# Kernel tuning notes

Measured on AMD Instinct MI355X. Metric: run time of the kernel, lower is better.

## Reference

```python
import jax, jax.numpy as jnp
import numpy as np

IN_FEATURES = 2048
OUT_FEATURES = 8192


def ternary_quantize(w):
    # BitNet 1.58b: scale = mean(|w|), round to {-1,0,1}, rescale
    scale = jnp.mean(jnp.abs(w)) + 1e-8
    w_q = jnp.clip(jnp.round(w / scale), -1.0, 1.0)
    return w_q * scale


def setup_inputs() -> dict:
    key = jax.random.key(0)
    kx, kw = jax.random.split(key)
    x = jax.random.normal(kx, (4, 2048, IN_FEATURES), dtype=jnp.float32)
    # nn.init.normal_(std=1/sqrt(in_features))
    weight = jax.random.normal(kw, (OUT_FEATURES, IN_FEATURES), dtype=jnp.float32) / np.sqrt(IN_FEATURES)
    return {"x": x, "weight": weight}


def reference(x, weight):
    w = ternary_quantize(weight)
    # F.linear: x @ w.T  -> [B, S, out_features]
    return jnp.einsum('bsd,od->bso', x, w)
```

## Files before the change

kernel.cpp:

```cpp
#include <hip/hip_runtime.h>
#include <hip/hip_bf16.h>
#include <stdint.h>


typedef __attribute__((ext_vector_type(8))) short   s16x8;
typedef __attribute__((ext_vector_type(4))) float   f32x4;

#define K_DIM   2048
#define K2      4096
#define N_DIM   8192
#define N4      4194304

__global__ void k_abs_part(const float4* __restrict__ w4, float* __restrict__ part) {
    int tid = blockIdx.x * 256 + threadIdx.x;
    float s = 0.f;
    for (int i = tid; i < N4; i += gridDim.x * 256) {
        float4 v = w4[i];
        s += fabsf(v.x) + fabsf(v.y) + fabsf(v.z) + fabsf(v.w);
    }
    for (int off = 32; off > 0; off >>= 1) s += __shfl_down(s, off, 64);
    __shared__ float tmp[4];
    int lane = threadIdx.x & 63, wid = threadIdx.x >> 6;
    if (lane == 0) tmp[wid] = s;
    __syncthreads();
    if (threadIdx.x == 0) part[blockIdx.x] = tmp[0] + tmp[1] + tmp[2] + tmp[3];
}

__global__ void k_abs_final(const float* __restrict__ part, float* __restrict__ scale) {
    float s = part[threadIdx.x] + part[threadIdx.x + 256] +
              part[threadIdx.x + 512] + part[threadIdx.x + 768];
    for (int off = 32; off > 0; off >>= 1) s += __shfl_down(s, off, 64);
    __shared__ float tmp[4];
    int lane = threadIdx.x & 63, wid = threadIdx.x >> 6;
    if (lane == 0) tmp[wid] = s;
    __syncthreads();
    if (threadIdx.x == 0) scale[0] = (tmp[0] + tmp[1] + tmp[2] + tmp[3]) / 16777216.0f + 1e-8f;
}

__device__ __forceinline__ uint32_t f2b(float f) {
    uint32_t u = __builtin_bit_cast(uint32_t, f);
    return (u + 0x7FFFu + ((u >> 16) & 1u)) >> 16;
}

__global__ void k_prep(const float4* __restrict__ w4, const float4* __restrict__ x4,
                       const float* __restrict__ scale_p,
                       uint2* __restrict__ wq, uint2* __restrict__ xb) {
    int tid = (blockIdx.x & 2047) * 256 + threadIdx.x;
    if (blockIdx.x < 2048) {
        const float sc = *scale_p;
        for (int i = tid; i < N4; i += 2048 * 256) {
            float4 v = w4[i];
            float q0 = rintf(v.x / sc), q1 = rintf(v.y / sc);
            float q2 = rintf(v.z / sc), q3 = rintf(v.w / sc);
            uint32_t b0 = (q0 == 0.f) ? 0u : (q0 > 0.f ? 0x3F80u : 0xBF80u);
            uint32_t b1 = (q1 == 0.f) ? 0u : (q1 > 0.f ? 0x3F80u : 0xBF80u);
            uint32_t b2 = (q2 == 0.f) ? 0u : (q2 > 0.f ? 0x3F80u : 0xBF80u);
            uint32_t b3 = (q3 == 0.f) ? 0u : (q3 > 0.f ? 0x3F80u : 0xBF80u);
            uint2 o; o.x = b0 | (b1 << 16); o.y = b2 | (b3 << 16);
            wq[i] = o;
        }
    } else {
        for (int i = tid; i < N4; i += 2048 * 256) {
            float4 v = x4[i];
            uint2 o;
            o.x = f2b(v.x) | (f2b(v.y) << 16);
            o.y = f2b(v.z) | (f2b(v.w) << 16);
            xb[i] = o;
        }
    }
}

__device__ __forceinline__ void mfma16(f32x4& c, s16x8 a, s16x8 b) {
    asm("v_mfma_f32_16x16x32_bf16 %0, %1, %2, %0" : "+v"(c) : "v"(a), "v"(b));
}
__device__ __forceinline__ void load_lds16(const void* g, void* l) {
    __builtin_amdgcn_global_load_lds(
        (const __attribute__((address_space(1))) uint32_t*)g,
        (__attribute__((address_space(3))) uint32_t*)l, 16, 0, 0);
}

#define SCHED0 __builtin_amdgcn_sched_barrier(0)
#define SBAR do { SCHED0; __builtin_amdgcn_s_barrier(); SCHED0; } while (0)
#define WAIT_VM(N) do { asm volatile("s_waitcnt vmcnt(" #N ")" ::: "memory"); SCHED0; } while (0)

#define C0 0
#define C1 65536

__global__ __launch_bounds__(512, 2) void k_gemm(
    const unsigned short* __restrict__ Xb,
    const unsigned short* __restrict__ Wb,
    const float* __restrict__ scale_p,
    float* __restrict__ out)
{
    extern __shared__ uint8_t smem[];
    const int tid  = threadIdx.x;
    const int lane = tid & 63;
    const int wid  = tid >> 6;
    const int wr   = wid >> 2;
    const int wc   = wid & 3;

    const int bid = blockIdx.x;
    const int xcd = bid & 7;
    const int l   = bid >> 3;
    const int tileRow = xcd * 4 + ((l >> 3) & 3);
    const int tileCol = (l >> 5) * 8 + (l & 7);

    const uint8_t* gA = (const uint8_t*)Xb + (size_t)tileRow * 256 * K2;
    const uint8_t* gB = (const uint8_t*)Wb + (size_t)tileCol * 256 * K2;

    const int srow = tid >> 3, sslot = tid & 7;
    const size_t srcOff = (size_t)srow * K2 + (size_t)((sslot ^ (srow & 7)) * 16);
    const uint8_t* gAs = gA + srcOff;
    const uint8_t* gBs = gB + srcOff;
    const int dstOff = tid * 16;

    const int rA = wr * 128 + (lane & 15);
    const int rB = wc * 64  + (lane & 15);
    const int h  = lane >> 4;
    const int pA0 = rA * 128 + (((h    ) ^ (rA & 7)) * 16);
    const int pA1 = rA * 128 + (((4 + h) ^ (rA & 7)) * 16);
    const int pB0 = rB * 128 + (((h    ) ^ (rB & 7)) * 16);
    const int pB1 = rB * 128 + (((4 + h) ^ (rB & 7)) * 16);

    s16x8 a[8][2], b[4][2];
    f32x4 acc[8][4];
    #pragma unroll
    for (int m = 0; m < 8; ++m)
        #pragma unroll
        for (int n = 0; n < 4; ++n) acc[m][n] = (f32x4){0.f, 0.f, 0.f, 0.f};

#define LD8(OFF) (*(const s16x8*)(smem + (OFF)))
#define STAGE(LBASE, GP, BOFF) do { \
    load_lds16((GP) + (BOFF),          smem + (LBASE) + dstOff); \
    load_lds16((GP) + (BOFF) + 262144, smem + (LBASE) + 8192 + dstOff); \
    SCHED0; } while (0)

#define RD_A03(AB) do { _Pragma("unroll") for (int m = 0; m < 4; ++m) { \
    a[m][0] = LD8((AB) + pA0 + m * 2048); a[m][1] = LD8((AB) + pA1 + m * 2048); } } while (0)
#define RD_A47(AB) do { _Pragma("unroll") for (int m = 4; m < 8; ++m) { \
    a[m][0] = LD8((AB) + pA0 + m * 2048); a[m][1] = LD8((AB) + pA1 + m * 2048); } } while (0)
#define RD_B01(AB) do { _Pragma("unroll") for (int n = 0; n < 2; ++n) { \
    b[n][0] = LD8((AB) + 32768 + pB0 + n * 2048); b[n][1] = LD8((AB) + 32768 + pB1 + n * 2048); } } while (0)
#define RD_B23(AB) do { _Pragma("unroll") for (int n = 2; n < 4; ++n) { \
    b[n][0] = LD8((AB) + 32768 + pB0 + n * 2048); b[n][1] = LD8((AB) + 32768 + pB1 + n * 2048); } } while (0)

#define MFMA_Q(MLO, NLO) do { \
    __builtin_amdgcn_s_setprio(1); \
    _Pragma("unroll") for (int kk = 0; kk < 2; ++kk) \
        _Pragma("unroll") for (int m = 0; m < 4; ++m) \
            _Pragma("unroll") for (int n = 0; n < 2; ++n) \
                mfma16(acc[(MLO) + m][(NLO) + n], a[(MLO) + m][kk], b[(NLO) + n][kk]); \
    __builtin_amdgcn_s_setprio(0); \
    SCHED0; } while (0)

    STAGE(C0,         gAs, 0);   STAGE(C0 + 16384, gAs, 524288);
    STAGE(C0 + 32768, gBs, 0);   STAGE(C0 + 49152, gBs, 524288);
    STAGE(C1,         gAs, 128); STAGE(C1 + 16384, gAs, 524288 + 128);
    STAGE(C1 + 32768, gBs, 128); STAGE(C1 + 49152, gBs, 524288 + 128);
    WAIT_VM(8);
    SBAR;

    #pragma unroll 1
    for (int i = 0; i < 15; ++i) {
        const int kb1 = (2 * i + 1) * 128;
        const int kb2 = kb1 + 128;
        const int kb3 = kb1 + 256;
        STAGE(C1 + 32768, gBs, kb1);
        RD_A03(C0); RD_B01(C0);
        MFMA_Q(0, 0);
        STAGE(C1 + 49152, gBs, 524288 + kb1);
        RD_A47(C0);
        MFMA_Q(4, 0);
        SBAR;
        STAGE(C0, gAs, kb2);
        RD_B23(C0);
        MFMA_Q(0, 2);
        STAGE(C0 + 16384, gAs, 524288 + kb2);
        MFMA_Q(4, 2);
        WAIT_VM(4); SBAR;
        STAGE(C0 + 32768, gBs, kb2);
        RD_A03(C1); RD_B01(C1);
        MFMA_Q(0, 0);
        STAGE(C0 + 49152, gBs, 524288 + kb2);
        RD_A47(C1);
        MFMA_Q(4, 0);
        SBAR;
        STAGE(C1, gAs, kb3);
        RD_B23(C1);
        MFMA_Q(0, 2);
        STAGE(C1 + 16384, gAs, 524288 + kb3);
        MFMA_Q(4, 2);
        WAIT_VM(4); SBAR;
    }

    {
        const int kb1 = 31 * 128;
        STAGE(C1 + 32768, gBs, kb1);
        RD_A03(C0); RD_B01(C0);
        MFMA_Q(0, 0);
        STAGE(C1 + 49152, gBs, 524288 + kb1);
        RD_A47(C0);
        MFMA_Q(4, 0);
        SBAR;
        RD_B23(C0);
        MFMA_Q(0, 2);
        MFMA_Q(4, 2);
        WAIT_VM(0); SBAR;
        RD_A03(C1); RD_B01(C1);
        MFMA_Q(0, 0);
        RD_A47(C1);
        MFMA_Q(4, 0);
        RD_B23(C1);
        MFMA_Q(0, 2);
        MFMA_Q(4, 2);
    }

    const float sc = *scale_p;
    const int orow0 = tileRow * 256 + wr * 128 + ((lane >> 4) << 2);
    const int ocol0 = tileCol * 256 + wc * 64 + (lane & 15);
    #pragma unroll
    for (int m = 0; m < 8; ++m)
        #pragma unroll
        for (int n = 0; n < 4; ++n)
            #pragma unroll
            for (int j = 0; j < 4; ++j)
                out[(size_t)(orow0 + m * 16 + j) * N_DIM + (ocol0 + n * 16)] = acc[m][n][j] * sc;

#undef LD8
#undef STAGE
#undef RD_A03
#undef RD_A47
#undef RD_B01
#undef RD_B23
#undef MFMA_Q
}

extern "C" void kernel_launch(void* const* d_in, const int* in_sizes, int n_in,
                              void* d_out, int out_size, void* d_ws, size_t ws_size,
                              hipStream_t stream) {
    const float* x = (const float*)d_in[0];
    const float* w = (const float*)d_in[1];
    float* out = (float*)d_out;
    uint8_t* ws = (uint8_t*)d_ws;

    float* part  = (float*)ws;
    float* scale = (float*)(ws + 4096);
    unsigned short* Xb = (unsigned short*)(ws + 8192);
    unsigned short* Wb = (unsigned short*)(ws + 8192 + 33554432ull);

    (void)hipFuncSetAttribute((const void*)k_gemm,
                              hipFuncAttributeMaxDynamicSharedMemorySize, 131072);

    hipLaunchKernelGGL(k_abs_part, dim3(1024), dim3(256), 0, stream, (const float4*)w, part);
    hipLaunchKernelGGL(k_abs_final, dim3(1), dim3(256), 0, stream, part, scale);
    hipLaunchKernelGGL(k_prep, dim3(4096), dim3(256), 0, stream,
                       (const float4*)w, (const float4*)x, scale, (uint2*)Wb, (uint2*)Xb);
    hipLaunchKernelGGL(k_gemm, dim3(1024), dim3(512), 131072, stream, Xb, Wb, scale, out);
}
```

Before: 277.8 us.

## Shrink GEMM block tile to 128x128 with 4 waves and 64KB LDS

```diff
diff --git a/kernel.cpp b/kernel.cpp
--- a/kernel.cpp
+++ b/kernel.cpp
@@ -83,10 +83,12 @@
 #define SBAR do { SCHED0; __builtin_amdgcn_s_barrier(); SCHED0; } while (0)
 #define WAIT_VM(N) do { asm volatile("s_waitcnt vmcnt(" #N ")" ::: "memory"); SCHED0; } while (0)
 
-#define C0 0
-#define C1 65536
-
-__global__ __launch_bounds__(512, 2) void k_gemm(
+#define A0B 0
+#define B0B 16384
+#define A1B 32768
+#define B1B 49152
+
+__global__ __launch_bounds__(256, 2) void k_gemm(
     const unsigned short* __restrict__ Xb,
     const unsigned short* __restrict__ Wb,
     const float* __restrict__ scale_p,
@@ -96,17 +98,17 @@
     const int tid  = threadIdx.x;
     const int lane = tid & 63;
     const int wid  = tid >> 6;
-    const int wr   = wid >> 2;
-    const int wc   = wid & 3;
+    const int wr   = wid >> 1;
+    const int wc   = wid & 1;
 
     const int bid = blockIdx.x;
     const int xcd = bid & 7;
     const int l   = bid >> 3;
-    const int tileRow = xcd * 4 + ((l >> 3) & 3);
-    const int tileCol = (l >> 5) * 8 + (l & 7);
-
-    const uint8_t* gA = (const uint8_t*)Xb + (size_t)tileRow * 256 * K2;
-    const uint8_t* gB = (const uint8_t*)Wb + (size_t)tileCol * 256 * K2;
+    const int tileRow = xcd * 8 + (l & 7);
+    const int tileCol = l >> 3;
+
+    const uint8_t* gA = (const uint8_t*)Xb + (size_t)tileRow * 128 * K2;
+    const uint8_t* gB = (const uint8_t*)Wb + (size_t)tileCol * 128 * K2;
 
     const int srow = tid >> 3, sslot = tid & 7;
     const size_t srcOff = (size_t)srow * K2 + (size_t)((sslot ^ (srow & 7)) * 16);
@@ -114,50 +116,46 @@
     const uint8_t* gBs = gB + srcOff;
     const int dstOff = tid * 16;
 
-    const int rA = wr * 128 + (lane & 15);
-    const int rB = wc * 64  + (lane & 15);
+    const int rA = wr * 64 + (lane & 15);
+    const int rB = wc * 64 + (lane & 15);
     const int h  = lane >> 4;
     const int pA0 = rA * 128 + (((h    ) ^ (rA & 7)) * 16);
     const int pA1 = rA * 128 + (((4 + h) ^ (rA & 7)) * 16);
     const int pB0 = rB * 128 + (((h    ) ^ (rB & 7)) * 16);
     const int pB1 = rB * 128 + (((4 + h) ^ (rB & 7)) * 16);
 
-    s16x8 a[8][2], b[4][2];
-    f32x4 acc[8][4];
+    s16x8 a[4][2], b[4][2];
+    f32x4 acc[4][4];
     #pragma unroll
-    for (int m = 0; m < 8; ++m)
+    for (int m = 0; m < 4; ++m)
         #pragma unroll
         for (int n = 0; n < 4; ++n) acc[m][n] = (f32x4){0.f, 0.f, 0.f, 0.f};
 
 #define LD8(OFF) (*(const s16x8*)(smem + (OFF)))
 #define STAGE(LBASE, GP, BOFF) do { \
     load_lds16((GP) + (BOFF),          smem + (LBASE) + dstOff); \
-    load_lds16((GP) + (BOFF) + 262144, smem + (LBASE) + 8192 + dstOff); \
+    load_lds16((GP) + (BOFF) + 131072, smem + (LBASE) + 4096 + dstOff); \
     SCHED0; } while (0)
 
-#define RD_A03(AB) do { _Pragma("unroll") for (int m = 0; m < 4; ++m) { \
+#define RD_A(AB) do { _Pragma("unroll") for (int m = 0; m < 4; ++m) { \
     a[m][0] = LD8((AB) + pA0 + m * 2048); a[m][1] = LD8((AB) + pA1 + m * 2048); } } while (0)
-#define RD_A47(AB) do { _Pragma("unroll") for (int m = 4; m < 8; ++m) { \
-    a[m][0] = LD8((AB) + pA0 + m * 2048); a[m][1] = LD8((AB) + pA1 + m * 2048); } } while (0)
-#define RD_B01(AB) do { _Pragma("unroll") for (int n = 0; n < 2; ++n) { \
-    b[n][0] = LD8((AB) + 32768 + pB0 + n * 2048); b[n][1] = LD8((AB) + 32768 + pB1 + n * 2048); } } while (0)
-#define RD_B23(AB) do { _Pragma("unroll") for (int n = 2; n < 4; ++n) { \
-    b[n][0] = LD8((AB) + 32768 + pB0 + n * 2048); b[n][1] = LD8((AB) + 32768 + pB1 + n * 2048); } } while (0)
-
-#define MFMA_Q(MLO, NLO) do { \
+#define RD_B01(BB) do { _Pragma("unroll") for (int n = 0; n < 2; ++n) { \
+    b[n][0] = LD8((BB) + pB0 + n * 2048); b[n][1] = LD8((BB) + pB1 + n * 2048); } } while (0)
+#define RD_B23(BB) do { _Pragma("unroll") for (int n = 2; n < 4; ++n) { \
+    b[n][0] = LD8((BB) + pB0 + n * 2048); b[n][1] = LD8((BB) + pB1 + n * 2048); } } while (0)
+
+#define MFMA_Q(NLO, KC) do { \
     __builtin_amdgcn_s_setprio(1); \
-    _Pragma("unroll") for (int kk = 0; kk < 2; ++kk) \
-        _Pragma("unroll") for (int m = 0; m < 4; ++m) \
-            _Pragma("unroll") for (int n = 0; n < 2; ++n) \
-                mfma16(acc[(MLO) + m][(NLO) + n], a[(MLO) + m][kk], b[(NLO) + n][kk]); \
+    _Pragma("unroll") for (int m = 0; m < 4; ++m) \
+        _Pragma("unroll") for (int n = 0; n < 2; ++n) \
+            mfma16(acc[m][(NLO) + n], a[m][(KC)], b[(NLO) + n][(KC)]); \
     __builtin_amdgcn_s_setprio(0); \
     SCHED0; } while (0)
 
-    STAGE(C0,         gAs, 0);   STAGE(C0 + 16384, gAs, 524288);
-    STAGE(C0 + 32768, gBs, 0);   STAGE(C0 + 49152, gBs, 524288);
-    STAGE(C1,         gAs, 128); STAGE(C1 + 16384, gAs, 524288 + 128);
-    STAGE(C1 + 32768, gBs, 128); STAGE(C1 + 49152, gBs, 524288 + 128);
-    WAIT_VM(8);
+    STAGE(A0B, gAs, 0);   STAGE(A0B + 8192, gAs, 262144);
+    STAGE(B0B, gBs, 0);   STAGE(B0B + 8192, gBs, 262144);
+    STAGE(A1B, gAs, 128); STAGE(A1B + 8192, gAs, 262144 + 128);
+    WAIT_VM(4);
     SBAR;
 
     #pragma unroll 1
@@ -165,61 +163,57 @@
         const int kb1 = (2 * i + 1) * 128;
         const int kb2 = kb1 + 128;
         const int kb3 = kb1 + 256;
-        STAGE(C1 + 32768, gBs, kb1);
-        RD_A03(C0); RD_B01(C0);
-        MFMA_Q(0, 0);
-        STAGE(C1 + 49152, gBs, 524288 + kb1);
-        RD_A47(C0);
-        MFMA_Q(4, 0);
+        STAGE(B1B, gBs, kb1);
+        RD_A(A0B); RD_B01(B0B);
+        MFMA_Q(0, 0);
+        STAGE(B1B + 8192, gBs, 262144 + kb1);
+        RD_B23(B0B);
+        MFMA_Q(0, 1);
         SBAR;
-        STAGE(C0, gAs, kb2);
-        RD_B23(C0);
-        MFMA_Q(0, 2);
-        STAGE(C0 + 16384, gAs, 524288 + kb2);
-        MFMA_Q(4, 2);
+        STAGE(A0B, gAs, kb2);
+        MFMA_Q(2, 0);
+        STAGE(A0B + 8192, gAs, 262144 + kb2);
+        MFMA_Q(2, 1);
         WAIT_VM(4); SBAR;
-        STAGE(C0 + 32768, gBs, kb2);
-        RD_A03(C1); RD_B01(C1);
-        MFMA_Q(0, 0);
-        STAGE(C0 + 49152, gBs, 524288 + kb2);
-        RD_A47(C1);
-        MFMA_Q(4, 0);
+        STAGE(B0B, gBs, kb2);
+        RD_A(A1B); RD_B01(B1B);
+        MFMA_Q(0, 0);
+        STAGE(B0B + 8192, gBs, 262144 + kb2);
+        RD_B23(B1B);
+        MFMA_Q(0, 1);
         SBAR;
-        STAGE(C1, gAs, kb3);
-        RD_B23(C1);
-        MFMA_Q(0, 2);
-        STAGE(C1 + 16384, gAs, 524288 + kb3);
-        MFMA_Q(4, 2);
+        STAGE(A1B, gAs, kb3);
+        MFMA_Q(2, 0);
+        STAGE(A1B + 8192, gAs, 262144 + kb3);
+        MFMA_Q(2, 1);
         WAIT_VM(4); SBAR;
     }
 
     {
         const int kb1 = 31 * 128;
-        STAGE(C1 + 32768, gBs, kb1);
-        RD_A03(C0); RD_B01(C0);
-        MFMA_Q(0, 0);
-        STAGE(C1 + 49152, gBs, 524288 + kb1);
-        RD_A47(C0);
-        MFMA_Q(4, 0);
+        STAGE(B1B, gBs, kb1);
+        RD_A(A0B); RD_B01(B0B);
+        MFMA_Q(0, 0);
+        STAGE(B1B + 8192, gBs, 262144 + kb1);
+        RD_B23(B0B);
+        MFMA_Q(0, 1);
         SBAR;
-        RD_B23(C0);
-        MFMA_Q(0, 2);
-        MFMA_Q(4, 2);
+        MFMA_Q(2, 0);
+        MFMA_Q(2, 1);
         WAIT_VM(0); SBAR;
-        RD_A03(C1); RD_B01(C1);
-        MFMA_Q(0, 0);
-        RD_A47(C1);
-        MFMA_Q(4, 0);
-        RD_B23(C1);
-        MFMA_Q(0, 2);
-        MFMA_Q(4, 2);
+        RD_A(A1B); RD_B01(B1B);
+        MFMA_Q(0, 0);
+        RD_B23(B1B);
+        MFMA_Q(0, 1);
+        MFMA_Q(2, 0);
+        MFMA_Q(2, 1);
     }
 
     const float sc = *scale_p;
-    const int orow0 = tileRow * 256 + wr * 128 + ((lane >> 4) << 2);
-    const int ocol0 = tileCol * 256 + wc * 64 + (lane & 15);
+    const int orow0 = tileRow * 128 + wr * 64 + ((lane >> 4) << 2);
+    const int ocol0 = tileCol * 128 + wc * 64 + (lane & 15);
     #pragma unroll
-    for (int m = 0; m < 8; ++m)
+    for (int m = 0; m < 4; ++m)
         #pragma unroll
         for (int n = 0; n < 4; ++n)
             #pragma unroll
@@ -228,8 +222,7 @@
 
 #undef LD8
 #undef STAGE
-#undef RD_A03
-#undef RD_A47
+#undef RD_A
 #undef RD_B01
 #undef RD_B23
 #undef MFMA_Q
@@ -249,11 +242,11 @@
     unsigned short* Wb = (unsigned short*)(ws + 8192 + 33554432ull);
 
     (void)hipFuncSetAttribute((const void*)k_gemm,
-                              hipFuncAttributeMaxDynamicSharedMemorySize, 131072);
+                              hipFuncAttributeMaxDynamicSharedMemorySize, 65536);
 
     hipLaunchKernelGGL(k_abs_part, dim3(1024), dim3(256), 0, stream, (const float4*)w, part);
     hipLaunchKernelGGL(k_abs_final, dim3(1), dim3(256), 0, stream, part, scale);
     hipLaunchKernelGGL(k_prep, dim3(4096), dim3(256), 0, stream,
                        (const float4*)w, (const float4*)x, scale, (uint2*)Wb, (uint2*)Xb);
-    hipLaunchKernelGGL(k_gemm, dim3(1024), dim3(512), 131072, stream, Xb, Wb, scale, out);
-}
+    hipLaunchKernelGGL(k_gemm, dim3(4096), dim3(256), 65536, stream, Xb, Wb, scale, out);
+}
```

New measurement: 312.2 us. 12.4% more time.
